# Performance work log

Hardware: AMD Instinct MI355X
Metric: run time of the kernel (lower is better)

Reference implementation:

```python
import jax, jax.numpy as jnp
import numpy as np

N = 100000
E = 1600000
F_IN = 128
HID = 16
HEADS = 8
NCLS = 2
NGRAPH = 64
NEG_SLOPE = 0.2


def setup_inputs() -> dict:
    key = jax.random.key(0)
    ks = jax.random.split(key, 12)
    x = jax.random.normal(ks[0], (N, F_IN), dtype=jnp.float32)
    edge_index = jax.random.randint(ks[1], (2, E), 0, N, dtype=jnp.int64)
    batch = jnp.sort(jax.random.randint(ks[2], (N,), 0, NGRAPH, dtype=jnp.int64))
    s1 = 1.0 / np.sqrt(F_IN)
    s2 = 1.0 / np.sqrt(HEADS * HID)
    W1 = jax.random.normal(ks[3], (F_IN, HEADS * HID), dtype=jnp.float32) * s1
    att_src1 = jax.random.normal(ks[4], (HEADS, HID), dtype=jnp.float32) * s2
    att_dst1 = jax.random.normal(ks[5], (HEADS, HID), dtype=jnp.float32) * s2
    b1 = jnp.zeros((HEADS * HID,), dtype=jnp.float32)
    W2 = jax.random.normal(ks[6], (HEADS * HID, 1 * NCLS), dtype=jnp.float32) * s2
    att_src2 = jax.random.normal(ks[7], (1, NCLS), dtype=jnp.float32)
    att_dst2 = jax.random.normal(ks[8], (1, NCLS), dtype=jnp.float32)
    b2 = jnp.zeros((NCLS,), dtype=jnp.float32)
    return {"x": x, "edge_index": edge_index, "batch": batch,
            "W1": W1, "att_src1": att_src1, "att_dst1": att_dst1, "b1": b1,
            "W2": W2, "att_src2": att_src2, "att_dst2": att_dst2, "b2": b2}


def _gat_conv(x, src, dst, W, att_src, att_dst, bias, heads, out_dim, concat):
    # x: [N, Fin]; src/dst: [E'] (self-loops already appended)
    h = (x @ W).reshape(N, heads, out_dim)              # [N, H, D]
    a_src = jnp.sum(h * att_src[None], axis=-1)          # [N, H]
    a_dst = jnp.sum(h * att_dst[None], axis=-1)          # [N, H]
    e = a_src[src] + a_dst[dst]                          # [E', H]
    e = jnp.where(e >= 0, e, NEG_SLOPE * e)              # leaky_relu
    # softmax over incoming edges of each destination node
    emax = jax.ops.segment_max(e, dst, num_segments=N)   # [N, H]
    ee = jnp.exp(e - emax[dst])
    denom = jax.ops.segment_sum(ee, dst, num_segments=N)
    alpha = ee / denom[dst]                              # [E', H]
    msg = h[src] * alpha[:, :, None]                     # [E', H, D]
    out = jax.ops.segment_sum(msg, dst, num_segments=N)  # [N, H, D]
    if concat:
        out = out.reshape(N, heads * out_dim)
    else:
        out = out.mean(axis=1)
    return out + bias


def reference(x, edge_index, batch, W1, att_src1, att_dst1, b1, W2, att_src2, att_dst2, b2):
    # add self-loops (PyG GATConv default add_self_loops=True)
    loop = jnp.arange(N, dtype=edge_index.dtype)
    src = jnp.concatenate([edge_index[0], loop])
    dst = jnp.concatenate([edge_index[1], loop])

    h = _gat_conv(x, src, dst, W1, att_src1, att_dst1, b1, HEADS, HID, True)
    h = jax.nn.elu(h)
    h = _gat_conv(h, src, dst, W2, att_src2, att_dst2, b2, 1, NCLS, False)

    # global mean pool over graphs
    ssum = jax.ops.segment_sum(h, batch, num_segments=NGRAPH)          # [G, C]
    cnt = jax.ops.segment_sum(jnp.ones((N,), h.dtype), batch, num_segments=NGRAPH)
    pooled = ssum / jnp.maximum(cnt, 1.0)[:, None]
    return jax.nn.log_softmax(pooled, axis=1)
```

## Files before the change

kernel.cpp:

```cpp
#include <hip/hip_runtime.h>
#include <math.h>

typedef long long ll;
typedef unsigned int u32;
typedef unsigned short u16;
typedef __attribute__((ext_vector_type(8))) short short8;
typedef __attribute__((ext_vector_type(4))) float f32x4;

#define NBLK 256
#define MAXBUK 512
#define CHUNK_MAX 8192

__device__ __forceinline__ int load_idx(const void* p, int i, int is64) {
  return is64 ? (int)((const ll*)p)[i] : ((const int*)p)[i];
}

__device__ __forceinline__ u16 f2bf(float f) {
  u32 u = __float_as_uint(f);
  u += 0x7FFFu + ((u >> 16) & 1u);
  return (u16)(u >> 16);
}

__global__ __launch_bounds__(256) void prep_kernel(
    const void* __restrict__ eidx, int ne2, const void* __restrict__ batch, int nb,
    const float* __restrict__ W1, u16* __restrict__ Wtb,
    float* __restrict__ pool, int* __restrict__ flags) {
  int blk = blockIdx.x, t = threadIdx.x;
  if (blk < 64) {
    int g = blk * 256 + t;
    int k = g >> 7, j = g & 127;
    Wtb[j * 128 + k] = f2bf(W1[g]);
  } else {
    if (t < 192) pool[t] = 0.f;
    ll v = 0;
    if (t < 16) {
      int i = (int)((ll)(t + 1) * (ne2 / 2 - 1) / 16);
      v = ((const ll*)eidx)[i];
    } else if (t < 32) {
      int i = (int)((ll)(t - 15) * (nb / 2 - 1) / 16);
      v = ((const ll*)batch)[i];
    }
    bool bad = (v < 0 || v >= (1LL << 31));
    unsigned long long mask = __ballot(bad);
    if (t == 0) {
      flags[0] = (mask & 0xFFFFull) ? 0 : 1;
      flags[1] = (mask & 0xFFFF0000ull) ? 0 : 1;
    }
  }
}

__global__ __launch_bounds__(256) void gemm1_kernel(
    const float* __restrict__ x, const u16* __restrict__ Wtb,
    const float* __restrict__ att_src, const float* __restrict__ att_dst,
    u16* __restrict__ h, float* __restrict__ a_src, float* __restrict__ a_dst,
    int nn) {
  __shared__ __align__(16) char smem[64 * 136 * 2 + 128 * 136 * 2];
  u16* xs = (u16*)smem;
  u16* Wt = (u16*)(smem + 64 * 136 * 2);
  float* hs = (float*)smem;
  int t = threadIdx.x;
  int n0 = blockIdx.x * 64;

  const uint4* W4 = (const uint4*)Wtb;
  #pragma unroll
  for (int p = 0; p < 8; ++p) {
    int i = t + p * 256;
    int j = i >> 4, kc = (i & 15) * 8;
    *(uint4*)&Wt[j * 136 + kc] = W4[i];
  }
  #pragma unroll
  for (int p = 0; p < 4; ++p) {
    int row = p * 16 + (t >> 4);
    int c = t & 15;
    int gn = n0 + row;
    uint4 pk = make_uint4(0u, 0u, 0u, 0u);
    if (gn < nn) {
      const float4* xp = (const float4*)(x + (size_t)gn * 128 + c * 8);
      float4 f0 = xp[0], f1 = xp[1];
      pk.x = (u32)f2bf(f0.x) | ((u32)f2bf(f0.y) << 16);
      pk.y = (u32)f2bf(f0.z) | ((u32)f2bf(f0.w) << 16);
      pk.z = (u32)f2bf(f1.x) | ((u32)f2bf(f1.y) << 16);
      pk.w = (u32)f2bf(f1.z) | ((u32)f2bf(f1.w) << 16);
    }
    *(uint4*)&xs[row * 136 + c * 8] = pk;
  }
  __syncthreads();

  int lane = t & 63, wid = t >> 6;
  int lrow = lane & 15, lq = lane >> 4;
  short8 a[4];
  #pragma unroll
  for (int ks = 0; ks < 4; ++ks) {
    int row = wid * 16 + lrow;
    a[ks] = *(const short8*)&xs[row * 136 + ks * 32 + lq * 8];
  }
  f32x4 c[8];
  #pragma unroll
  for (int jt = 0; jt < 8; ++jt) c[jt] = (f32x4)(0.f);
  #pragma unroll
  for (int jt = 0; jt < 8; ++jt) {
    int j = jt * 16 + lrow;
    #pragma unroll
    for (int ks = 0; ks < 4; ++ks) {
      short8 b = *(const short8*)&Wt[j * 136 + ks * 32 + lq * 8];
      c[jt] = __builtin_amdgcn_mfma_f32_16x16x32_bf16(a[ks], b, c[jt], 0, 0, 0);
    }
  }
  __syncthreads();

  #pragma unroll
  for (int jt = 0; jt < 8; ++jt) {
    #pragma unroll
    for (int r = 0; r < 4; ++r) {
      hs[(wid * 16 + lq * 4 + r) * 132 + jt * 16 + lrow] = c[jt][r];
    }
  }
  __syncthreads();

  int q = t & 31, p = t >> 5;
  const float4 as4 = ((const float4*)att_src)[q];
  const float4 ad4 = ((const float4*)att_dst)[q];
  int head = q >> 2;
  #pragma unroll
  for (int rr = 0; rr < 8; ++rr) {
    int row = rr * 8 + p;
    int n = n0 + row;
    float4 v = *(const float4*)&hs[row * 132 + q * 4];
    float s = v.x * as4.x + v.y * as4.y + v.z * as4.z + v.w * as4.w;
    float d = v.x * ad4.x + v.y * ad4.y + v.z * ad4.z + v.w * ad4.w;
    s += __shfl_xor(s, 1); s += __shfl_xor(s, 2);
    d += __shfl_xor(d, 1); d += __shfl_xor(d, 2);
    if (n < nn) {
      uint2 pk;
      pk.x = (u32)f2bf(v.x) | ((u32)f2bf(v.y) << 16);
      pk.y = (u32)f2bf(v.z) | ((u32)f2bf(v.w) << 16);
      ((uint2*)(h + (size_t)n * 128))[q] = pk;
      if ((q & 3) == 0) { a_src[n * 8 + head] = s; a_dst[n * 8 + head] = d; }
    }
  }
}

__global__ __launch_bounds__(512) void ehist_kernel(
    const void* __restrict__ eidx, int E, int EP, int chunk,
    const int* __restrict__ flags, int* __restrict__ hist_g, int nbuk) {
  __shared__ int cnt[MAXBUK];
  int t = threadIdx.x, blk = blockIdx.x;
  if (t < MAXBUK) cnt[t] = 0;
  __syncthreads();
  int lo = blk * chunk, hi = min(lo + chunk, EP);
  int is64 = flags[0];
  for (int i = lo + t; i < hi; i += 512) {
    int d = (i < E) ? load_idx(eidx, E + i, is64) : (i - E);
    atomicAdd(&cnt[d >> 8], 1);
  }
  __syncthreads();
  if (t < nbuk) hist_g[t * NBLK + blk] = cnt[t];
}

__global__ __launch_bounds__(256) void scan_blk(const int* __restrict__ in,
                                                int* __restrict__ out,
                                                int* __restrict__ bsums, int n) {
  int t = threadIdx.x;
  int i = blockIdx.x * 256 + t;
  int v = (i < n) ? in[i] : 0;
  int lane = t & 63, w = t >> 6;
  int s = v;
  #pragma unroll
  for (int off = 1; off < 64; off <<= 1) {
    int u = __shfl_up(s, off);
    if (lane >= off) s += u;
  }
  __shared__ int wsum[4];
  if (lane == 63) wsum[w] = s;
  __syncthreads();
  int add = 0;
  for (int k = 0; k < w; ++k) add += wsum[k];
  int incl = s + add;
  if (i < n) out[i] = incl - v;
  if (t == 255) bsums[blockIdx.x] = incl;
}

__global__ __launch_bounds__(1024) void scan_top(int* __restrict__ bsums, int nb) {
  int t = threadIdx.x;
  int v = (t < nb) ? bsums[t] : 0;
  int lane = t & 63, w = t >> 6;
  int s = v;
  #pragma unroll
  for (int off = 1; off < 64; off <<= 1) {
    int u = __shfl_up(s, off);
    if (lane >= off) s += u;
  }
  __shared__ int ws[16];
  if (lane == 63) ws[w] = s;
  __syncthreads();
  int add = 0;
  for (int k = 0; k < w; ++k) add += ws[k];
  if (t < nb) bsums[t] = s + add - v;
}

__global__ __launch_bounds__(512) void escatter_kernel(
    const void* __restrict__ eidx, int E, int EP, int chunk,
    const int* __restrict__ flags, const int* __restrict__ hist_g,
    const int* __restrict__ pbase, const int* __restrict__ bsums,
    u32* __restrict__ pairs, int nbuk) {
  __shared__ int cnt[MAXBUK];
  __shared__ int lbase[MAXBUK];
  __shared__ int lcur[MAXBUK];
  __shared__ u32 buf[CHUNK_MAX];
  __shared__ int wsum[8];
  int t = threadIdx.x, blk = blockIdx.x;
  int v = 0;
  if (t < nbuk) { v = hist_g[t * NBLK + blk]; cnt[t] = v; }
  int lane = t & 63, w = t >> 6;
  int s = v;
  #pragma unroll
  for (int off = 1; off < 64; off <<= 1) {
    int u = __shfl_up(s, off);
    if (lane >= off) s += u;
  }
  if (lane == 63) wsum[w] = s;
  __syncthreads();
  int add = 0;
  for (int k = 0; k < w; ++k) add += wsum[k];
  if (t < nbuk) { lbase[t] = s + add - v; lcur[t] = s + add - v; }
  __syncthreads();
  int lo = blk * chunk, hi = min(lo + chunk, EP);
  int is64 = flags[0];
  for (int i = lo + t; i < hi; i += 512) {
    int sv, d;
    if (i < E) { sv = load_idx(eidx, i, is64); d = load_idx(eidx, E + i, is64); }
    else { sv = d = i - E; }
    int pos = atomicAdd(&lcur[d >> 8], 1);
    buf[pos] = ((u32)(d & 255) << 24) | (u32)sv;
  }
  __syncthreads();
  for (int b = w; b < nbuk; b += 8) {
    int n_b = cnt[b];
    int lb = lbase[b];
    int gb = pbase[b * NBLK + blk] + bsums[b];
    for (int k = lane; k < n_b; k += 64) {
      pairs[gb + k] = buf[lb + k];
    }
  }
}

__global__ __launch_bounds__(256) void bfinal_kernel(
    const u32* __restrict__ pairs, const int* __restrict__ pbase,
    const int* __restrict__ bsums,
    int* __restrict__ offs, int* __restrict__ ends, int* __restrict__ ssrc,
    int N, int EP, int nbuk) {
  int b = blockIdx.x, t = threadIdx.x;
  int nb0 = b << 8;
  __shared__ int cnt[256];
  __shared__ int cur[256];
  __shared__ int wsum[4];
  cnt[t] = 0;
  __syncthreads();
  int seg_start = pbase[b * NBLK] + bsums[b];
  int seg_end = (b + 1 < nbuk) ? (pbase[(b + 1) * NBLK] + bsums[b + 1]) : EP;
  for (int i = seg_start + t; i < seg_end; i += 256) {
    atomicAdd(&cnt[pairs[i] >> 24], 1);
  }
  __syncthreads();
  int v = cnt[t];
  int lane = t & 63, w = t >> 6;
  int s = v;
  #pragma unroll
  for (int off = 1; off < 64; off <<= 1) {
    int u = __shfl_up(s, off);
    if (lane >= off) s += u;
  }
  if (lane == 63) wsum[w] = s;
  __syncthreads();
  int add = 0;
  for (int k = 0; k < w; ++k) add += wsum[k];
  int excl = s + add - v;
  cur[t] = excl;
  int node = nb0 + t;
  if (node < N) { offs[node] = seg_start + excl; ends[node] = seg_start + excl + v; }
  __syncthreads();
  for (int i = seg_start + t; i < seg_end; i += 256) {
    u32 p = pairs[i];
    int pos = atomicAdd(&cur[p >> 24], 1);
    ssrc[seg_start + pos] = (int)(p & 0xFFFFFFu);
  }
}

__global__ __launch_bounds__(256) void node1_kernel(
    const int* __restrict__ ssrc, const int* __restrict__ offs, const int* __restrict__ ends,
    const u16* __restrict__ h, const float* __restrict__ a_src, const float* __restrict__ a_dst,
    const float* __restrict__ b1, const float* __restrict__ W2,
    const float* __restrict__ att_s2, const float* __restrict__ att_d2,
    float4* __restrict__ rec, int nn) {
  int t = threadIdx.x;
  int wid = t >> 6, lane = t & 63;
  int grp = lane >> 4, lg = lane & 15;
  int n = blockIdx.x * 16 + wid * 4 + grp;
  bool nvalid = (n < nn);
  int nc = nvalid ? n : (nn - 1);
  int hh = lg >> 1;
  float adst = a_dst[nc * 8 + hh];
  int beg = offs[nc], end = ends[nc];
  int deg = nvalid ? (end - beg) : 0;
  int maxd = deg;
  maxd = max(maxd, __shfl_xor(maxd, 16));
  maxd = max(maxd, __shfl_xor(maxd, 32));
  float acc[8];
  #pragma unroll
  for (int k = 0; k < 8; ++k) acc[k] = 0.f;
  float dsum = 0.f;
  const u32* h32 = (const u32*)h;
  for (int it = 0; it < maxd; it += 4) {
    int s4[4]; float ea4[4]; uint4 v4[4];
    #pragma unroll
    for (int u = 0; u < 4; ++u) {
      int id = beg + it + u;
      s4[u] = ssrc[id < end ? id : end - 1];
    }
    #pragma unroll
    for (int u = 0; u < 4; ++u) {
      v4[u]  = *(const uint4*)(h32 + s4[u] * 64 + lg * 4);
      ea4[u] = a_src[s4[u] * 8 + hh];
    }
    #pragma unroll
    for (int u = 0; u < 4; ++u) {
      float e = ea4[u] + adst;
      e = fmaxf(e, 0.2f * e);
      float ee = (it + u < deg) ? __expf(e) : 0.f;
      dsum += ee;
      acc[0] = fmaf(ee, __uint_as_float(v4[u].x << 16),          acc[0]);
      acc[1] = fmaf(ee, __uint_as_float(v4[u].x & 0xFFFF0000u),  acc[1]);
      acc[2] = fmaf(ee, __uint_as_float(v4[u].y << 16),          acc[2]);
      acc[3] = fmaf(ee, __uint_as_float(v4[u].y & 0xFFFF0000u),  acc[3]);
      acc[4] = fmaf(ee, __uint_as_float(v4[u].z << 16),          acc[4]);
      acc[5] = fmaf(ee, __uint_as_float(v4[u].z & 0xFFFF0000u),  acc[5]);
      acc[6] = fmaf(ee, __uint_as_float(v4[u].w << 16),          acc[6]);
      acc[7] = fmaf(ee, __uint_as_float(v4[u].w & 0xFFFF0000u),  acc[7]);
    }
  }
  float inv = 1.f / dsum;
  float p0 = 0.f, p1 = 0.f;
  #pragma unroll
  for (int k = 0; k < 8; ++k) {
    int j = lg * 8 + k;
    float o = acc[k] * inv + b1[j];
    o = (o > 0.f) ? o : expm1f(o);
    p0 = fmaf(o, W2[j * 2],     p0);
    p1 = fmaf(o, W2[j * 2 + 1], p1);
  }
  #pragma unroll
  for (int m = 1; m < 16; m <<= 1) { p0 += __shfl_xor(p0, m); p1 += __shfl_xor(p1, m); }
  if (nvalid && lg == 0) {
    rec[n] = make_float4(p0, p1,
                         p0 * att_s2[0] + p1 * att_s2[1],
                         p0 * att_d2[0] + p1 * att_d2[1]);
  }
}

__global__ __launch_bounds__(256) void node2_kernel(
    const int* __restrict__ ssrc, const int* __restrict__ offs, const int* __restrict__ ends,
    const float4* __restrict__ rec, const float* __restrict__ b2,
    const void* __restrict__ batch, const int* __restrict__ flags,
    float* __restrict__ pool, int nn) {
  __shared__ float psum[128];
  __shared__ float pcnt[64];
  int t = threadIdx.x;
  if (t < 128) psum[t] = 0.f;
  if (t < 64) pcnt[t] = 0.f;
  __syncthreads();
  int grp = t >> 3, lane8 = t & 7;
  int b64 = flags[1];
  int n = blockIdx.x * 32 + grp;
  if (n < nn) {
    float adst = rec[n].w;
    int beg = offs[n], end = ends[n];
    float acc0 = 0.f, acc1 = 0.f, dsum = 0.f;
    for (int idx = beg + lane8; idx < end; idx += 8) {
      int s = ssrc[idx];
      float4 r = rec[s];
      float e = r.z + adst;
      e = (e < 0.f) ? 0.2f * e : e;
      float ee = __expf(e);
      acc0 = fmaf(ee, r.x, acc0);
      acc1 = fmaf(ee, r.y, acc1);
      dsum += ee;
    }
    #pragma unroll
    for (int m = 1; m < 8; m <<= 1) {
      acc0 += __shfl_xor(acc0, m);
      acc1 += __shfl_xor(acc1, m);
      dsum += __shfl_xor(dsum, m);
    }
    if (lane8 == 0) {
      float o0 = acc0 / dsum + b2[0];
      float o1 = acc1 / dsum + b2[1];
      int g = load_idx(batch, n, b64);
      atomicAdd(&psum[g * 2], o0);
      atomicAdd(&psum[g * 2 + 1], o1);
      atomicAdd(&pcnt[g], 1.f);
    }
  }
  __syncthreads();
  if (t < 64 && pcnt[t] > 0.f) {
    atomicAdd(&pool[t * 2], psum[t * 2]);
    atomicAdd(&pool[t * 2 + 1], psum[t * 2 + 1]);
    atomicAdd(&pool[128 + t], pcnt[t]);
  }
}

__global__ void finalize_kernel(const float* __restrict__ pool, float* __restrict__ out) {
  int g = threadIdx.x;
  if (g < 64) {
    float c = fmaxf(pool[128 + g], 1.f);
    float p0 = pool[g * 2] / c, p1 = pool[g * 2 + 1] / c;
    float m = fmaxf(p0, p1);
    float lse = m + logf(expf(p0 - m) + expf(p1 - m));
    out[g * 2] = p0 - lse;
    out[g * 2 + 1] = p1 - lse;
  }
}

extern "C" void kernel_launch(void* const* d_in, const int* in_sizes, int n_in,
                              void* d_out, int out_size, void* d_ws, size_t ws_size,
                              hipStream_t stream) {
  const float* x        = (const float*)d_in[0];
  const void* eidx      = d_in[1];
  const void* batch     = d_in[2];
  const float* W1       = (const float*)d_in[3];
  const float* att_src1 = (const float*)d_in[4];
  const float* att_dst1 = (const float*)d_in[5];
  const float* b1       = (const float*)d_in[6];
  const float* W2       = (const float*)d_in[7];
  const float* att_src2 = (const float*)d_in[8];
  const float* att_dst2 = (const float*)d_in[9];
  const float* b2       = (const float*)d_in[10];
  float* out = (float*)d_out;

  int N = in_sizes[0] / 128;
  int E = in_sizes[1] / 2;
  int EP = E + N;
  int NBUK = (N + 255) >> 8;
  int NC = NBUK * NBLK;
  int chunk = (((EP + NBLK - 1) / NBLK) + 1) & ~1;

  char* ws = (char*)d_ws;
  size_t o = 0;
  auto alloc = [&](size_t bytes) -> void* {
    void* p = ws + o;
    o += (bytes + 255) & ~(size_t)255;
    return p;
  };
  u16*   h      = (u16*)alloc((size_t)N * 128 * 2);
  u16*   Wtb    = (u16*)alloc(128 * 128 * 2);
  float* a_src1 = (float*)alloc((size_t)N * 8 * 4);
  float* a_dst1 = (float*)alloc((size_t)N * 8 * 4);
  int*   offs   = (int*)alloc((size_t)N * 4);
  int*   ends   = (int*)alloc((size_t)N * 4);
  int*   hist_g = (int*)alloc((size_t)NC * 4);
  int*   pbase  = (int*)alloc((size_t)NC * 4);
  int*   bsums  = (int*)alloc((size_t)(NBUK + 1) * 4);
  u32*   pairs  = (u32*)alloc((size_t)EP * 4);
  int*   ssrc   = (int*)alloc((size_t)EP * 4);
  float4* rec   = (float4*)alloc((size_t)N * 16);
  float* pool   = (float*)alloc(192 * 4);
  int*   flags  = (int*)alloc(2 * 4);

  prep_kernel<<<65, 256, 0, stream>>>(eidx, 2 * E, batch, N, W1, Wtb, pool, flags);
  gemm1_kernel<<<(N + 63) / 64, 256, 0, stream>>>(x, Wtb, att_src1, att_dst1,
                                                  h, a_src1, a_dst1, N);
  ehist_kernel<<<NBLK, 512, 0, stream>>>(eidx, E, EP, chunk, flags, hist_g, NBUK);
  scan_blk<<<NBUK, 256, 0, stream>>>(hist_g, pbase, bsums, NC);
  scan_top<<<1, 1024, 0, stream>>>(bsums, NBUK);
  escatter_kernel<<<NBLK, 512, 0, stream>>>(eidx, E, EP, chunk, flags, hist_g,
                                            pbase, bsums, pairs, NBUK);
  bfinal_kernel<<<NBUK, 256, 0, stream>>>(pairs, pbase, bsums, offs, ends, ssrc,
                                          N, EP, NBUK);
  node1_kernel<<<(N + 15) / 16, 256, 0, stream>>>(ssrc, offs, ends, h, a_src1, a_dst1,
                                                  b1, W2, att_src2, att_dst2,
                                                  rec, N);
  node2_kernel<<<(N + 31) / 32, 256, 0, stream>>>(ssrc, offs, ends, rec,
                                                  b2, batch, flags, pool, N);
  finalize_kernel<<<1, 64, 0, stream>>>(pool, out);
}
```

Before: 205.0 us.

## Fuse per-bucket CSR finalization into node kernels via shared-memory edge lists

Drops the separate bfinal kernel and the global offs/ends/ssrc arrays. Each node kernel block now takes half of a 256-node bucket, counts and scatters that bucket's packed pairs into a shared-memory source list, then runs the aggregation from LDS. This removes one launch and the global write and re-read of the sorted source array. In exchange, each block rescans the whole bucket's pairs in both node kernels, and there are fewer, larger blocks using more LDS. Edge lists longer than the fixed shared buffer are silently truncated.

```diff
diff --git a/kernel.cpp b/kernel.cpp
--- a/kernel.cpp
+++ b/kernel.cpp
@@ -10,6 +10,7 @@
 #define NBLK 256
 #define MAXBUK 512
 #define CHUNK_MAX 8192
+#define SBUF 5120
 
 __device__ __forceinline__ int load_idx(const void* p, int i, int is64) {
   return is64 ? (int)((const ll*)p)[i] : ((const int*)p)[i];
@@ -244,160 +245,214 @@
   }
 }
 
-__global__ __launch_bounds__(256) void bfinal_kernel(
-    const u32* __restrict__ pairs, const int* __restrict__ pbase,
-    const int* __restrict__ bsums,
-    int* __restrict__ offs, int* __restrict__ ends, int* __restrict__ ssrc,
-    int N, int EP, int nbuk) {
-  int b = blockIdx.x, t = threadIdx.x;
-  int nb0 = b << 8;
-  __shared__ int cnt[256];
-  __shared__ int cur[256];
-  __shared__ int wsum[4];
-  cnt[t] = 0;
-  __syncthreads();
-  int seg_start = pbase[b * NBLK] + bsums[b];
-  int seg_end = (b + 1 < nbuk) ? (pbase[(b + 1) * NBLK] + bsums[b + 1]) : EP;
-  for (int i = seg_start + t; i < seg_end; i += 256) {
-    atomicAdd(&cnt[pairs[i] >> 24], 1);
-  }
-  __syncthreads();
-  int v = cnt[t];
-  int lane = t & 63, w = t >> 6;
-  int s = v;
-  #pragma unroll
-  for (int off = 1; off < 64; off <<= 1) {
-    int u = __shfl_up(s, off);
-    if (lane >= off) s += u;
-  }
-  if (lane == 63) wsum[w] = s;
-  __syncthreads();
-  int add = 0;
-  for (int k = 0; k < w; ++k) add += wsum[k];
-  int excl = s + add - v;
-  cur[t] = excl;
-  int node = nb0 + t;
-  if (node < N) { offs[node] = seg_start + excl; ends[node] = seg_start + excl + v; }
-  __syncthreads();
-  for (int i = seg_start + t; i < seg_end; i += 256) {
-    u32 p = pairs[i];
-    int pos = atomicAdd(&cur[p >> 24], 1);
-    ssrc[seg_start + pos] = (int)(p & 0xFFFFFFu);
-  }
-}
-
-__global__ __launch_bounds__(256) void node1_kernel(
-    const int* __restrict__ ssrc, const int* __restrict__ offs, const int* __restrict__ ends,
+__global__ __launch_bounds__(512) void node1_kernel(
+    const u32* __restrict__ pairs, const int* __restrict__ bsums,
     const u16* __restrict__ h, const float* __restrict__ a_src, const float* __restrict__ a_dst,
     const float* __restrict__ b1, const float* __restrict__ W2,
     const float* __restrict__ att_s2, const float* __restrict__ att_d2,
-    float4* __restrict__ rec, int nn) {
+    float4* __restrict__ rec, int N, int EP, int nbuk) {
+  __shared__ int lcnt[128], lofs[128], lcur[128];
+  __shared__ int wsum[2];
+  __shared__ u32 sbuf[SBUF];
+  int blk = blockIdx.x;
+  int b = blk >> 1, hbase = (blk & 1) << 7;
   int t = threadIdx.x;
+  if (t < 128) lcnt[t] = 0;
+  __syncthreads();
+  int seg_start = bsums[b];
+  int seg_end = (b + 1 < nbuk) ? bsums[b + 1] : EP;
+  for (int i = seg_start + t; i < seg_end; i += 512) {
+    int ld = (int)(pairs[i] >> 24);
+    if ((ld & 128) == hbase) atomicAdd(&lcnt[ld & 127], 1);
+  }
+  __syncthreads();
+  int v = 0, sincl = 0;
+  if (t < 128) {
+    v = lcnt[t];
+    sincl = v;
+    #pragma unroll
+    for (int off = 1; off < 64; off <<= 1) {
+      int u = __shfl_up(sincl, off);
+      if ((t & 63) >= off) sincl += u;
+    }
+    if ((t & 63) == 63) wsum[t >> 6] = sincl;
+  }
+  __syncthreads();
+  if (t < 128) {
+    int add = (t >= 64) ? wsum[0] : 0;
+    int excl = sincl + add - v;
+    lofs[t] = excl; lcur[t] = excl;
+  }
+  __syncthreads();
+  for (int i = seg_start + t; i < seg_end; i += 512) {
+    u32 p = pairs[i];
+    int ld = (int)(p >> 24);
+    if ((ld & 128) == hbase) {
+      int pos = atomicAdd(&lcur[ld & 127], 1);
+      if (pos < SBUF) sbuf[pos] = p & 0xFFFFFFu;
+    }
+  }
+  __syncthreads();
+
   int wid = t >> 6, lane = t & 63;
   int grp = lane >> 4, lg = lane & 15;
-  int n = blockIdx.x * 16 + wid * 4 + grp;
-  bool nvalid = (n < nn);
-  int nc = nvalid ? n : (nn - 1);
   int hh = lg >> 1;
-  float adst = a_dst[nc * 8 + hh];
-  int beg = offs[nc], end = ends[nc];
-  int deg = nvalid ? (end - beg) : 0;
-  int maxd = deg;
-  maxd = max(maxd, __shfl_xor(maxd, 16));
-  maxd = max(maxd, __shfl_xor(maxd, 32));
-  float acc[8];
-  #pragma unroll
-  for (int k = 0; k < 8; ++k) acc[k] = 0.f;
-  float dsum = 0.f;
   const u32* h32 = (const u32*)h;
-  for (int it = 0; it < maxd; it += 4) {
-    int s4[4]; float ea4[4]; uint4 v4[4];
+  #pragma unroll 1
+  for (int pass = 0; pass < 4; ++pass) {
+    int ln = pass * 32 + wid * 4 + grp;
+    int n = (b << 8) + hbase + ln;
+    bool nvalid = (n < N);
+    int beg = 0, deg = 0;
+    if (nvalid) {
+      beg = lofs[ln]; deg = lcnt[ln];
+      if (beg >= SBUF) deg = 0; else deg = min(deg, SBUF - beg);
+    }
+    int maxd = deg;
+    maxd = max(maxd, __shfl_xor(maxd, 16));
+    maxd = max(maxd, __shfl_xor(maxd, 32));
+    float adst = nvalid ? a_dst[n * 8 + hh] : 0.f;
+    float acc[8];
     #pragma unroll
-    for (int u = 0; u < 4; ++u) {
-      int id = beg + it + u;
-      s4[u] = ssrc[id < end ? id : end - 1];
-    }
-    #pragma unroll
-    for (int u = 0; u < 4; ++u) {
-      v4[u]  = *(const uint4*)(h32 + s4[u] * 64 + lg * 4);
-      ea4[u] = a_src[s4[u] * 8 + hh];
-    }
-    #pragma unroll
-    for (int u = 0; u < 4; ++u) {
-      float e = ea4[u] + adst;
-      e = fmaxf(e, 0.2f * e);
-      float ee = (it + u < deg) ? __expf(e) : 0.f;
-      dsum += ee;
-      acc[0] = fmaf(ee, __uint_as_float(v4[u].x << 16),          acc[0]);
-      acc[1] = fmaf(ee, __uint_as_float(v4[u].x & 0xFFFF0000u),  acc[1]);
-      acc[2] = fmaf(ee, __uint_as_float(v4[u].y << 16),          acc[2]);
-      acc[3] = fmaf(ee, __uint_as_float(v4[u].y & 0xFFFF0000u),  acc[3]);
-      acc[4] = fmaf(ee, __uint_as_float(v4[u].z << 16),          acc[4]);
-      acc[5] = fmaf(ee, __uint_as_float(v4[u].z & 0xFFFF0000u),  acc[5]);
-      acc[6] = fmaf(ee, __uint_as_float(v4[u].w << 16),          acc[6]);
-      acc[7] = fmaf(ee, __uint_as_float(v4[u].w & 0xFFFF0000u),  acc[7]);
-    }
-  }
-  float inv = 1.f / dsum;
-  float p0 = 0.f, p1 = 0.f;
-  #pragma unroll
-  for (int k = 0; k < 8; ++k) {
-    int j = lg * 8 + k;
-    float o = acc[k] * inv + b1[j];
-    o = (o > 0.f) ? o : expm1f(o);
-    p0 = fmaf(o, W2[j * 2],     p0);
-    p1 = fmaf(o, W2[j * 2 + 1], p1);
-  }
-  #pragma unroll
-  for (int m = 1; m < 16; m <<= 1) { p0 += __shfl_xor(p0, m); p1 += __shfl_xor(p1, m); }
-  if (nvalid && lg == 0) {
-    rec[n] = make_float4(p0, p1,
-                         p0 * att_s2[0] + p1 * att_s2[1],
-                         p0 * att_d2[0] + p1 * att_d2[1]);
-  }
-}
-
-__global__ __launch_bounds__(256) void node2_kernel(
-    const int* __restrict__ ssrc, const int* __restrict__ offs, const int* __restrict__ ends,
+    for (int k = 0; k < 8; ++k) acc[k] = 0.f;
+    float dsum = 0.f;
+    for (int it = 0; it < maxd; it += 4) {
+      int s4[4]; float ea4[4]; uint4 v4[4];
+      #pragma unroll
+      for (int u = 0; u < 4; ++u) {
+        int id = it + u;
+        int cl = (id < deg) ? id : (deg > 0 ? deg - 1 : 0);
+        s4[u] = (deg > 0) ? (int)sbuf[beg + cl] : 0;
+      }
+      #pragma unroll
+      for (int u = 0; u < 4; ++u) {
+        v4[u]  = *(const uint4*)(h32 + s4[u] * 64 + lg * 4);
+        ea4[u] = a_src[s4[u] * 8 + hh];
+      }
+      #pragma unroll
+      for (int u = 0; u < 4; ++u) {
+        float e = ea4[u] + adst;
+        e = fmaxf(e, 0.2f * e);
+        float ee = (it + u < deg) ? __expf(e) : 0.f;
+        dsum += ee;
+        acc[0] = fmaf(ee, __uint_as_float(v4[u].x << 16),          acc[0]);
+        acc[1] = fmaf(ee, __uint_as_float(v4[u].x & 0xFFFF0000u),  acc[1]);
+        acc[2] = fmaf(ee, __uint_as_float(v4[u].y << 16),          acc[2]);
+        acc[3] = fmaf(ee, __uint_as_float(v4[u].y & 0xFFFF0000u),  acc[3]);
+        acc[4] = fmaf(ee, __uint_as_float(v4[u].z << 16),          acc[4]);
+        acc[5] = fmaf(ee, __uint_as_float(v4[u].z & 0xFFFF0000u),  acc[5]);
+        acc[6] = fmaf(ee, __uint_as_float(v4[u].w << 16),          acc[6]);
+        acc[7] = fmaf(ee, __uint_as_float(v4[u].w & 0xFFFF0000u),  acc[7]);
+      }
+    }
+    if (nvalid && deg > 0) {
+      float inv = 1.f / dsum;
+      float p0 = 0.f, p1 = 0.f;
+      #pragma unroll
+      for (int k = 0; k < 8; ++k) {
+        int j = lg * 8 + k;
+        float o = acc[k] * inv + b1[j];
+        o = (o > 0.f) ? o : expm1f(o);
+        p0 = fmaf(o, W2[j * 2],     p0);
+        p1 = fmaf(o, W2[j * 2 + 1], p1);
+      }
+      #pragma unroll
+      for (int m = 1; m < 16; m <<= 1) { p0 += __shfl_xor(p0, m); p1 += __shfl_xor(p1, m); }
+      if (lg == 0) {
+        rec[n] = make_float4(p0, p1,
+                             p0 * att_s2[0] + p1 * att_s2[1],
+                             p0 * att_d2[0] + p1 * att_d2[1]);
+      }
+    }
+  }
+}
+
+__global__ __launch_bounds__(512) void node2_kernel(
+    const u32* __restrict__ pairs, const int* __restrict__ bsums,
     const float4* __restrict__ rec, const float* __restrict__ b2,
     const void* __restrict__ batch, const int* __restrict__ flags,
-    float* __restrict__ pool, int nn) {
+    float* __restrict__ pool, int N, int EP, int nbuk) {
+  __shared__ int lcnt[128], lofs[128], lcur[128];
+  __shared__ int wsum[2];
+  __shared__ u32 sbuf[SBUF];
   __shared__ float psum[128];
   __shared__ float pcnt[64];
+  int blk = blockIdx.x;
+  int b = blk >> 1, hbase = (blk & 1) << 7;
   int t = threadIdx.x;
-  if (t < 128) psum[t] = 0.f;
+  if (t < 128) { lcnt[t] = 0; psum[t] = 0.f; }
   if (t < 64) pcnt[t] = 0.f;
   __syncthreads();
+  int seg_start = bsums[b];
+  int seg_end = (b + 1 < nbuk) ? bsums[b + 1] : EP;
+  for (int i = seg_start + t; i < seg_end; i += 512) {
+    int ld = (int)(pairs[i] >> 24);
+    if ((ld & 128) == hbase) atomicAdd(&lcnt[ld & 127], 1);
+  }
+  __syncthreads();
+  int v = 0, sincl = 0;
+  if (t < 128) {
+    v = lcnt[t];
+    sincl = v;
+    #pragma unroll
+    for (int off = 1; off < 64; off <<= 1) {
+      int u = __shfl_up(sincl, off);
+      if ((t & 63) >= off) sincl += u;
+    }
+    if ((t & 63) == 63) wsum[t >> 6] = sincl;
+  }
+  __syncthreads();
+  if (t < 128) {
+    int add = (t >= 64) ? wsum[0] : 0;
+    int excl = sincl + add - v;
+    lofs[t] = excl; lcur[t] = excl;
+  }
+  __syncthreads();
+  for (int i = seg_start + t; i < seg_end; i += 512) {
+    u32 p = pairs[i];
+    int ld = (int)(p >> 24);
+    if ((ld & 128) == hbase) {
+      int pos = atomicAdd(&lcur[ld & 127], 1);
+      if (pos < SBUF) sbuf[pos] = p & 0xFFFFFFu;
+    }
+  }
+  __syncthreads();
+
   int grp = t >> 3, lane8 = t & 7;
   int b64 = flags[1];
-  int n = blockIdx.x * 32 + grp;
-  if (n < nn) {
-    float adst = rec[n].w;
-    int beg = offs[n], end = ends[n];
-    float acc0 = 0.f, acc1 = 0.f, dsum = 0.f;
-    for (int idx = beg + lane8; idx < end; idx += 8) {
-      int s = ssrc[idx];
-      float4 r = rec[s];
-      float e = r.z + adst;
-      e = (e < 0.f) ? 0.2f * e : e;
-      float ee = __expf(e);
-      acc0 = fmaf(ee, r.x, acc0);
-      acc1 = fmaf(ee, r.y, acc1);
-      dsum += ee;
-    }
-    #pragma unroll
-    for (int m = 1; m < 8; m <<= 1) {
-      acc0 += __shfl_xor(acc0, m);
-      acc1 += __shfl_xor(acc1, m);
-      dsum += __shfl_xor(dsum, m);
-    }
-    if (lane8 == 0) {
-      float o0 = acc0 / dsum + b2[0];
-      float o1 = acc1 / dsum + b2[1];
-      int g = load_idx(batch, n, b64);
-      atomicAdd(&psum[g * 2], o0);
-      atomicAdd(&psum[g * 2 + 1], o1);
-      atomicAdd(&pcnt[g], 1.f);
+  #pragma unroll 1
+  for (int pass = 0; pass < 2; ++pass) {
+    int ln = pass * 64 + grp;
+    int n = (b << 8) + hbase + ln;
+    if (n < N) {
+      int beg = lofs[ln], deg = lcnt[ln];
+      if (beg >= SBUF) deg = 0; else deg = min(deg, SBUF - beg);
+      float adst = rec[n].w;
+      float acc0 = 0.f, acc1 = 0.f, dsum = 0.f;
+      for (int idx = lane8; idx < deg; idx += 8) {
+        int s = (int)sbuf[beg + idx];
+        float4 r = rec[s];
+        float e = r.z + adst;
+        e = (e < 0.f) ? 0.2f * e : e;
+        float ee = __expf(e);
+        acc0 = fmaf(ee, r.x, acc0);
+        acc1 = fmaf(ee, r.y, acc1);
+        dsum += ee;
+      }
+      #pragma unroll
+      for (int m = 1; m < 8; m <<= 1) {
+        acc0 += __shfl_xor(acc0, m);
+        acc1 += __shfl_xor(acc1, m);
+        dsum += __shfl_xor(dsum, m);
+      }
+      if (lane8 == 0 && deg > 0) {
+        float o0 = acc0 / dsum + b2[0];
+        float o1 = acc1 / dsum + b2[1];
+        int g = load_idx(batch, n, b64);
+        atomicAdd(&psum[g * 2], o0);
+        atomicAdd(&psum[g * 2 + 1], o1);
+        atomicAdd(&pcnt[g], 1.f);
+      }
     }
   }
   __syncthreads();
@@ -440,6 +495,7 @@
   int E = in_sizes[1] / 2;
   int EP = E + N;
   int NBUK = (N + 255) >> 8;
+  int NHB  = (N + 127) >> 7;
   int NC = NBUK * NBLK;
   int chunk = (((EP + NBLK - 1) / NBLK) + 1) & ~1;
 
@@ -454,13 +510,10 @@
   u16*   Wtb    = (u16*)alloc(128 * 128 * 2);
   float* a_src1 = (float*)alloc((size_t)N * 8 * 4);
   float* a_dst1 = (float*)alloc((size_t)N * 8 * 4);
-  int*   offs   = (int*)alloc((size_t)N * 4);
-  int*   ends   = (int*)alloc((size_t)N * 4);
   int*   hist_g = (int*)alloc((size_t)NC * 4);
   int*   pbase  = (int*)alloc((size_t)NC * 4);
   int*   bsums  = (int*)alloc((size_t)(NBUK + 1) * 4);
   u32*   pairs  = (u32*)alloc((size_t)EP * 4);
-  int*   ssrc   = (int*)alloc((size_t)EP * 4);
   float4* rec   = (float4*)alloc((size_t)N * 16);
   float* pool   = (float*)alloc(192 * 4);
   int*   flags  = (int*)alloc(2 * 4);
@@ -473,12 +526,10 @@
   scan_top<<<1, 1024, 0, stream>>>(bsums, NBUK);
   escatter_kernel<<<NBLK, 512, 0, stream>>>(eidx, E, EP, chunk, flags, hist_g,
                                             pbase, bsums, pairs, NBUK);
-  bfinal_kernel<<<NBUK, 256, 0, stream>>>(pairs, pbase, bsums, offs, ends, ssrc,
-                                          N, EP, NBUK);
-  node1_kernel<<<(N + 15) / 16, 256, 0, stream>>>(ssrc, offs, ends, h, a_src1, a_dst1,
-                                                  b1, W2, att_src2, att_dst2,
-                                                  rec, N);
-  node2_kernel<<<(N + 31) / 32, 256, 0, stream>>>(ssrc, offs, ends, rec,
-                                                  b2, batch, flags, pool, N);
+  node1_kernel<<<NHB, 512, 0, stream>>>(pairs, bsums, h, a_src1, a_dst1,
+                                        b1, W2, att_src2, att_dst2,
+                                        rec, N, EP, NBUK);
+  node2_kernel<<<NHB, 512, 0, stream>>>(pairs, bsums, rec, b2, batch, flags,
+                                        pool, N, EP, NBUK);
   finalize_kernel<<<1, 64, 0, stream>>>(pool, out);
 }
```

Result: no change. 203.6 us (-0.7%).
